# Kernel tuning notes

Measured on AMD Instinct MI355X. Metric: run time of the kernel, lower is better.

The kernel has to match this reference:

```python
import jax, jax.numpy as jnp
import numpy as np

NUM_USERS = 100000
NUM_ITEMS = 50000
N_NODES = NUM_USERS + NUM_ITEMS
LATENT_DIM = 64
XIJ_DIM = 16
N_LAYERS = 3
NNZ = 6400000
BATCH = 8192


def setup_inputs() -> dict:
    key = jax.random.key(0)
    ks = jax.random.split(key, 12)
    return {
        "emb_user": jax.random.normal(ks[0], (NUM_USERS, LATENT_DIM), jnp.float32),
        "emb_item": jax.random.normal(ks[1], (NUM_ITEMS, LATENT_DIM), jnp.float32),
        "emb_user_xij": jax.random.normal(ks[2], (NUM_USERS, XIJ_DIM), jnp.float32),
        "emb_item_xij1": jax.random.normal(ks[3], (NUM_ITEMS, XIJ_DIM), jnp.float32),
        "emb_item_xij0": jax.random.normal(ks[4], (NUM_ITEMS, XIJ_DIM), jnp.float32),
        "w_user": jax.random.normal(ks[5], (1,), jnp.float32),
        "w_item": jax.random.normal(ks[6], (1,), jnp.float32),
        "graph_vals": jax.random.uniform(ks[7], (NNZ,), jnp.float32),
        "graph_rows": jax.random.randint(ks[8], (NNZ,), 0, N_NODES, jnp.int64).astype(jnp.int32),
        "graph_cols": jax.random.randint(ks[9], (NNZ,), 0, N_NODES, jnp.int64).astype(jnp.int32),
        "users": jax.random.randint(ks[10], (BATCH,), 0, NUM_USERS, jnp.int64).astype(jnp.int32),
        "items": jax.random.randint(ks[11], (BATCH,), 0, NUM_ITEMS, jnp.int64).astype(jnp.int32),
        "xij": jax.random.randint(jax.random.fold_in(key, 99), (BATCH,), 0, 2, jnp.int32),
    }


def _spmm(rows, cols, vals, x):
    # y[r] = sum_{e: rows[e]==r} vals[e] * x[cols[e]]
    return jax.ops.segment_sum(vals[:, None] * x[cols], rows, num_segments=N_NODES)


def reference(emb_user, emb_item, emb_user_xij, emb_item_xij1, emb_item_xij0,
              w_user, w_item, graph_vals, graph_rows, graph_cols,
              users, items, xij):
    # LightGCN propagation with running-mean accumulator (fuses the stack+mean)
    all_emb = jnp.concatenate([emb_user, emb_item], axis=0)  # [N, D]
    acc = all_emb
    for _ in range(N_LAYERS):
        all_emb = _spmm(graph_rows, graph_cols, graph_vals, all_emb)
        acc = acc + all_emb
    light_out = acc / (N_LAYERS + 1)
    all_users = light_out[:NUM_USERS]
    all_items = light_out[NUM_USERS:]

    users_emb = w_user * all_users[users]          # [B, D]
    items_emb = w_item * all_items[items]          # [B, D]
    xij_user_emb = emb_user_xij[users]             # [B, Dx]
    xij_item_emb = jnp.where(xij[:, None].astype(bool),
                             emb_item_xij1[items], emb_item_xij0[items])

    users_mix = jax.nn.softmax(jnp.concatenate([users_emb, xij_user_emb], axis=1), axis=1)
    items_mix = jax.nn.sigmoid(jnp.concatenate([items_emb, xij_item_emb], axis=1))
    gamma = jnp.sum(users_mix * items_mix, axis=1)  # [B]
    return gamma
```

## Files before the change

kernel.cpp:

```cpp
#include <hip/hip_runtime.h>
#include <hip/hip_bf16.h>
#include <hip/hip_fp16.h>
#include <math.h>

#define NUM_USERS 100000
#define NUM_ITEMS 50000
#define N_NODES   150000
#define DIM       64
#define VAL_SCALE 16383.0f
#define VAL_INV   (1.0f / 16383.0f)

#define SSHIFT 9
#define SROWS  512
#define NBS    ((N_NODES + SROWS - 1) / SROWS)
#define CAP    17
#define FLUSH  8
#define SCAT_WGS 1280
#define GPAD   16
#define SLOTS  32768
#define PKSLOTS 22744
#define SENTINEL 0xFFFFFFFFu
#define BBT 512

__global__ void copy_init_kernel(const float4* __restrict__ eu, const float4* __restrict__ ei,
                                 ushort4* __restrict__ cur, int total4) {
    int i = blockIdx.x * blockDim.x + threadIdx.x;
    if (i >= total4) return;
    const int user_lim = NUM_USERS * (DIM / 4);
    float4 v = (i < user_lim) ? eu[i] : ei[i - user_lim];
    ushort4 h;
    h.x = __half_as_ushort(__float2half_rn(v.x));
    h.y = __half_as_ushort(__float2half_rn(v.y));
    h.z = __half_as_ushort(__float2half_rn(v.z));
    h.w = __half_as_ushort(__float2half_rn(v.w));
    cur[i] = h;
}

__global__ void gcur_init_kernel(int* __restrict__ gcur) {
    int b = blockIdx.x * blockDim.x + threadIdx.x;
    if (b < NBS) gcur[b * GPAD] = b * SLOTS;
}

__global__ __launch_bounds__(256) void binned_scatter_kernel(
        const int* __restrict__ rows, const int* __restrict__ cols,
        const float* __restrict__ vals, int* __restrict__ gcur,
        uint2* __restrict__ pk8, int nnz) {
    __shared__ unsigned       lbufA[NBS * CAP];
    __shared__ unsigned short lbufB[NBS * CAP];
    __shared__ int            lcur[NBS];
    int t = threadIdx.x;
    for (int i = t; i < NBS; i += 256) lcur[i] = 0;
    __syncthreads();

    int per_wg = (((nnz + (int)gridDim.x - 1) / (int)gridDim.x) + 1) & ~1;
    int e0 = blockIdx.x * per_wg;
    int e1 = min(e0 + per_wg, nnz);

    #define PROC(rr, cc, vv) { \
        int r = (rr); \
        unsigned q = __float2uint_rn((vv) * VAL_SCALE); \
        unsigned ax = (unsigned)(cc) | (q << 18); \
        int b = r >> SSHIFT; \
        int pos = atomicAdd(&lcur[b], 1); \
        if (pos < CAP) { \
            lbufA[b * CAP + pos] = ax; \
            lbufB[b * CAP + pos] = (unsigned short)(r - (b << SSHIFT)); \
        } else { \
            atomicSub(&lcur[b], 1); \
            int p = atomicAdd(&gcur[b * GPAD], 8); \
            *(uint4*)(&pk8[p])     = make_uint4(ax, (unsigned)r, 0u, SENTINEL); \
            *(uint4*)(&pk8[p + 2]) = make_uint4(0u, SENTINEL, 0u, SENTINEL); \
            *(uint4*)(&pk8[p + 4]) = make_uint4(0u, SENTINEL, 0u, SENTINEL); \
            *(uint4*)(&pk8[p + 6]) = make_uint4(0u, SENTINEL, 0u, SENTINEL); \
        } }

    for (int base = e0; base < e1; base += 512) {
        int e = base + t * 2;
        if (e + 1 < e1) {
            int2   r2 = *(const int2*)(rows + e);
            int2   c2 = *(const int2*)(cols + e);
            float2 v2 = *(const float2*)(vals + e);
            PROC(r2.x, c2.x, v2.x)
            PROC(r2.y, c2.y, v2.y)
        } else if (e < e1) {
            PROC(rows[e], cols[e], vals[e])
        }
        __syncthreads();
        for (int b2 = t; b2 < NBS; b2 += 256) {
            int c = lcur[b2];
            if (c >= FLUSH) {
                int ng = c >> 3;
                int p = atomicAdd(&gcur[b2 * GPAD], ng * 8);
                unsigned rbase = (unsigned)(b2 << SSHIFT);
                for (int j = 0; j < ng * 8; j += 2) {
                    uint4 q = make_uint4(lbufA[b2 * CAP + j],     rbase + lbufB[b2 * CAP + j],
                                         lbufA[b2 * CAP + j + 1], rbase + lbufB[b2 * CAP + j + 1]);
                    *(uint4*)(&pk8[p + j]) = q;
                }
                int rem = c - ng * 8;
                for (int j = 0; j < rem; ++j) {
                    lbufA[b2 * CAP + j] = lbufA[b2 * CAP + ng * 8 + j];
                    lbufB[b2 * CAP + j] = lbufB[b2 * CAP + ng * 8 + j];
                }
                lcur[b2] = rem;
            }
        }
        __syncthreads();
    }
    for (int b2 = t; b2 < NBS; b2 += 256) {
        int c = lcur[b2];
        if (c > 0) {
            int p = atomicAdd(&gcur[b2 * GPAD], 8);
            unsigned rbase = (unsigned)(b2 << SSHIFT);
            for (int j = 0; j < 8; j += 2) {
                unsigned a0 = (j     < c) ? lbufA[b2 * CAP + j]             : 0u;
                unsigned b0 = (j     < c) ? rbase + lbufB[b2 * CAP + j]     : SENTINEL;
                unsigned a1 = (j + 1 < c) ? lbufA[b2 * CAP + j + 1]         : 0u;
                unsigned b1 = (j + 1 < c) ? rbase + lbufB[b2 * CAP + j + 1] : SENTINEL;
                *(uint4*)(&pk8[p + j]) = make_uint4(a0, b0, a1, b1);
            }
        }
    }
}

__global__ __launch_bounds__(BBT) void bucket_build_kernel(const int* __restrict__ gcur,
                                                           const uint2* __restrict__ pk8,
                                                           unsigned* __restrict__ pk,
                                                           int* __restrict__ rowbeg,
                                                           int* __restrict__ rowend) {
    __shared__ int lc[SROWS];
    __shared__ int ps[SROWS];
    int b  = blockIdx.x;
    int r0 = b * SROWS;
    int nr = min(r0 + SROWS, N_NODES) - r0;
    int t  = threadIdx.x;
    lc[t] = 0;
    __syncthreads();

    const uint4* p4 = (const uint4*)pk8;
    int i0   = (b * SLOTS) >> 1;
    int iend = gcur[b * GPAD] >> 1;

    #define CNT(q) { \
        if ((q).y != SENTINEL) atomicAdd(&lc[(int)(q).y - r0], 1); \
        if ((q).w != SENTINEL) atomicAdd(&lc[(int)(q).w - r0], 1); }

    int i = i0 + t;
    for (; i + 3 * BBT < iend; i += 4 * BBT) {
        uint4 qa = p4[i], qb = p4[i + BBT], qc = p4[i + 2 * BBT], qd = p4[i + 3 * BBT];
        CNT(qa) CNT(qb) CNT(qc) CNT(qd)
    }
    for (; i < iend; i += BBT) { uint4 qa = p4[i]; CNT(qa) }
    __syncthreads();

    int c = lc[t];
    ps[t] = c;
    __syncthreads();
    #pragma unroll
    for (int off = 1; off < SROWS; off <<= 1) {
        int u = (t >= off) ? ps[t - off] : 0;
        __syncthreads();
        ps[t] += u;
        __syncthreads();
    }
    int base = b * PKSLOTS + ps[t] - c;
    if (t < nr) { rowbeg[r0 + t] = base; rowend[r0 + t] = base + c; }
    lc[t] = base;
    __syncthreads();

    #define PLC(q) { \
        if ((q).y != SENTINEL) { int p_ = atomicAdd(&lc[(int)(q).y - r0], 1); pk[p_] = (q).x; } \
        if ((q).w != SENTINEL) { int p_ = atomicAdd(&lc[(int)(q).w - r0], 1); pk[p_] = (q).z; } }

    i = i0 + t;
    for (; i + 3 * BBT < iend; i += 4 * BBT) {
        uint4 qa = p4[i], qb = p4[i + BBT], qc = p4[i + 2 * BBT], qd = p4[i + 3 * BBT];
        PLC(qa) PLC(qb) PLC(qc) PLC(qd)
    }
    for (; i < iend; i += BBT) { uint4 qa = p4[i]; PLC(qa) }
}

__device__ __forceinline__ float row_pull(const int* __restrict__ rowbeg,
                                          const int* __restrict__ rowend,
                                          const unsigned* __restrict__ pk,
                                          const __half* __restrict__ x,
                                          int row, int lane) {
    int s0 = rowbeg[row];
    int s1 = rowend[row];
    float acc = 0.f;
    int e = s0;
    for (; e + 16 <= s1; e += 16) {
        unsigned p0 = pk[e + 0],  p1 = pk[e + 1],  p2 = pk[e + 2],  p3 = pk[e + 3];
        unsigned p4 = pk[e + 4],  p5 = pk[e + 5],  p6 = pk[e + 6],  p7 = pk[e + 7];
        unsigned p8 = pk[e + 8],  p9 = pk[e + 9],  pA = pk[e + 10], pB = pk[e + 11];
        unsigned pC = pk[e + 12], pD = pk[e + 13], pE = pk[e + 14], pF = pk[e + 15];
        float x0 = __half2float(x[((p0 & 0x3FFFFu) << 6) + lane]);
        float x1 = __half2float(x[((p1 & 0x3FFFFu) << 6) + lane]);
        float x2 = __half2float(x[((p2 & 0x3FFFFu) << 6) + lane]);
        float x3 = __half2float(x[((p3 & 0x3FFFFu) << 6) + lane]);
        float x4 = __half2float(x[((p4 & 0x3FFFFu) << 6) + lane]);
        float x5 = __half2float(x[((p5 & 0x3FFFFu) << 6) + lane]);
        float x6 = __half2float(x[((p6 & 0x3FFFFu) << 6) + lane]);
        float x7 = __half2float(x[((p7 & 0x3FFFFu) << 6) + lane]);
        float x8 = __half2float(x[((p8 & 0x3FFFFu) << 6) + lane]);
        float x9 = __half2float(x[((p9 & 0x3FFFFu) << 6) + lane]);
        float xA = __half2float(x[((pA & 0x3FFFFu) << 6) + lane]);
        float xB = __half2float(x[((pB & 0x3FFFFu) << 6) + lane]);
        float xC = __half2float(x[((pC & 0x3FFFFu) << 6) + lane]);
        float xD = __half2float(x[((pD & 0x3FFFFu) << 6) + lane]);
        float xE = __half2float(x[((pE & 0x3FFFFu) << 6) + lane]);
        float xF = __half2float(x[((pF & 0x3FFFFu) << 6) + lane]);
        acc = fmaf((float)(p0 >> 18), x0, acc);
        acc = fmaf((float)(p1 >> 18), x1, acc);
        acc = fmaf((float)(p2 >> 18), x2, acc);
        acc = fmaf((float)(p3 >> 18), x3, acc);
        acc = fmaf((float)(p4 >> 18), x4, acc);
        acc = fmaf((float)(p5 >> 18), x5, acc);
        acc = fmaf((float)(p6 >> 18), x6, acc);
        acc = fmaf((float)(p7 >> 18), x7, acc);
        acc = fmaf((float)(p8 >> 18), x8, acc);
        acc = fmaf((float)(p9 >> 18), x9, acc);
        acc = fmaf((float)(pA >> 18), xA, acc);
        acc = fmaf((float)(pB >> 18), xB, acc);
        acc = fmaf((float)(pC >> 18), xC, acc);
        acc = fmaf((float)(pD >> 18), xD, acc);
        acc = fmaf((float)(pE >> 18), xE, acc);
        acc = fmaf((float)(pF >> 18), xF, acc);
    }
    for (; e + 8 <= s1; e += 8) {
        unsigned p0 = pk[e + 0], p1 = pk[e + 1], p2 = pk[e + 2], p3 = pk[e + 3];
        unsigned p4 = pk[e + 4], p5 = pk[e + 5], p6 = pk[e + 6], p7 = pk[e + 7];
        float x0 = __half2float(x[((p0 & 0x3FFFFu) << 6) + lane]);
        float x1 = __half2float(x[((p1 & 0x3FFFFu) << 6) + lane]);
        float x2 = __half2float(x[((p2 & 0x3FFFFu) << 6) + lane]);
        float x3 = __half2float(x[((p3 & 0x3FFFFu) << 6) + lane]);
        float x4 = __half2float(x[((p4 & 0x3FFFFu) << 6) + lane]);
        float x5 = __half2float(x[((p5 & 0x3FFFFu) << 6) + lane]);
        float x6 = __half2float(x[((p6 & 0x3FFFFu) << 6) + lane]);
        float x7 = __half2float(x[((p7 & 0x3FFFFu) << 6) + lane]);
        acc = fmaf((float)(p0 >> 18), x0, acc);
        acc = fmaf((float)(p1 >> 18), x1, acc);
        acc = fmaf((float)(p2 >> 18), x2, acc);
        acc = fmaf((float)(p3 >> 18), x3, acc);
        acc = fmaf((float)(p4 >> 18), x4, acc);
        acc = fmaf((float)(p5 >> 18), x5, acc);
        acc = fmaf((float)(p6 >> 18), x6, acc);
        acc = fmaf((float)(p7 >> 18), x7, acc);
    }
    for (; e < s1; ++e) {
        unsigned p = pk[e];
        acc = fmaf((float)(p >> 18), __half2float(x[((p & 0x3FFFFu) << 6) + lane]), acc);
    }
    return acc * VAL_INV;
}

__device__ __forceinline__ float pull_range(const unsigned* __restrict__ pk,
                                            const __half* __restrict__ x,
                                            int e, int s1, int lane, float acc) {
    for (; e + 8 <= s1; e += 8) {
        unsigned p0 = pk[e + 0], p1 = pk[e + 1], p2 = pk[e + 2], p3 = pk[e + 3];
        unsigned p4 = pk[e + 4], p5 = pk[e + 5], p6 = pk[e + 6], p7 = pk[e + 7];
        float x0 = __half2float(x[((p0 & 0x3FFFFu) << 6) + lane]);
        float x1 = __half2float(x[((p1 & 0x3FFFFu) << 6) + lane]);
        float x2 = __half2float(x[((p2 & 0x3FFFFu) << 6) + lane]);
        float x3 = __half2float(x[((p3 & 0x3FFFFu) << 6) + lane]);
        float x4 = __half2float(x[((p4 & 0x3FFFFu) << 6) + lane]);
        float x5 = __half2float(x[((p5 & 0x3FFFFu) << 6) + lane]);
        float x6 = __half2float(x[((p6 & 0x3FFFFu) << 6) + lane]);
        float x7 = __half2float(x[((p7 & 0x3FFFFu) << 6) + lane]);
        acc = fmaf((float)(p0 >> 18), x0, acc);
        acc = fmaf((float)(p1 >> 18), x1, acc);
        acc = fmaf((float)(p2 >> 18), x2, acc);
        acc = fmaf((float)(p3 >> 18), x3, acc);
        acc = fmaf((float)(p4 >> 18), x4, acc);
        acc = fmaf((float)(p5 >> 18), x5, acc);
        acc = fmaf((float)(p6 >> 18), x6, acc);
        acc = fmaf((float)(p7 >> 18), x7, acc);
    }
    for (; e < s1; ++e) {
        unsigned p = pk[e];
        acc = fmaf((float)(p >> 18), __half2float(x[((p & 0x3FFFFu) << 6) + lane]), acc);
    }
    return acc;
}

__global__ __launch_bounds__(256) void pull_kernel(const int* __restrict__ rowbeg,
                                                   const int* __restrict__ rowend,
                                                   const unsigned* __restrict__ pk,
                                                   const __half* __restrict__ x,
                                                   __half* __restrict__ y) {
    int lane = threadIdx.x & 63;
    int wv   = __builtin_amdgcn_readfirstlane(threadIdx.x >> 6);
    int row  = blockIdx.x * 4 + wv;
    if (row >= N_NODES) return;
    float acc = row_pull(rowbeg, rowend, pk, x, row, lane);
    y[((size_t)row << 6) + lane] = __float2half_rn(acc);
}

__global__ __launch_bounds__(256) void tail_kernel(const int* __restrict__ rowbeg,
                                                   const int* __restrict__ rowend,
                                                   const unsigned* __restrict__ pk,
                                                   const __half* __restrict__ cur,
                                                   const __half* __restrict__ nxt,
                                                   const float* __restrict__ eu,
                                                   const float* __restrict__ ei,
                                                   const float* __restrict__ exu,
                                                   const float* __restrict__ exi1,
                                                   const float* __restrict__ exi0,
                                                   const float* __restrict__ w_user,
                                                   const float* __restrict__ w_item,
                                                   const int* __restrict__ users,
                                                   const int* __restrict__ items,
                                                   const int* __restrict__ xijf,
                                                   float* __restrict__ out, int batch) {
    int lane = threadIdx.x & 63;
    int wv   = blockIdx.x * 4 + __builtin_amdgcn_readfirstlane(threadIdx.x >> 6);
    if (wv >= batch) return;
    int u    = users[wv];
    int it   = items[wv];
    int xf   = xijf[wv];
    int rowU = u;
    int rowI = NUM_USERS + it;

    int eA = rowbeg[rowU], sA = rowend[rowU];
    int eB = rowbeg[rowI], sB = rowend[rowI];
    float aU = 0.f, aI = 0.f;
    for (; eA + 8 <= sA && eB + 8 <= sB; eA += 8, eB += 8) {
        unsigned a0 = pk[eA + 0], a1 = pk[eA + 1], a2 = pk[eA + 2], a3 = pk[eA + 3];
        unsigned a4 = pk[eA + 4], a5 = pk[eA + 5], a6 = pk[eA + 6], a7 = pk[eA + 7];
        unsigned b0 = pk[eB + 0], b1 = pk[eB + 1], b2 = pk[eB + 2], b3 = pk[eB + 3];
        unsigned b4 = pk[eB + 4], b5 = pk[eB + 5], b6 = pk[eB + 6], b7 = pk[eB + 7];
        float xa0 = __half2float(cur[((a0 & 0x3FFFFu) << 6) + lane]);
        float xa1 = __half2float(cur[((a1 & 0x3FFFFu) << 6) + lane]);
        float xa2 = __half2float(cur[((a2 & 0x3FFFFu) << 6) + lane]);
        float xa3 = __half2float(cur[((a3 & 0x3FFFFu) << 6) + lane]);
        float xa4 = __half2float(cur[((a4 & 0x3FFFFu) << 6) + lane]);
        float xa5 = __half2float(cur[((a5 & 0x3FFFFu) << 6) + lane]);
        float xa6 = __half2float(cur[((a6 & 0x3FFFFu) << 6) + lane]);
        float xa7 = __half2float(cur[((a7 & 0x3FFFFu) << 6) + lane]);
        float xb0 = __half2float(cur[((b0 & 0x3FFFFu) << 6) + lane]);
        float xb1 = __half2float(cur[((b1 & 0x3FFFFu) << 6) + lane]);
        float xb2 = __half2float(cur[((b2 & 0x3FFFFu) << 6) + lane]);
        float xb3 = __half2float(cur[((b3 & 0x3FFFFu) << 6) + lane]);
        float xb4 = __half2float(cur[((b4 & 0x3FFFFu) << 6) + lane]);
        float xb5 = __half2float(cur[((b5 & 0x3FFFFu) << 6) + lane]);
        float xb6 = __half2float(cur[((b6 & 0x3FFFFu) << 6) + lane]);
        float xb7 = __half2float(cur[((b7 & 0x3FFFFu) << 6) + lane]);
        aU = fmaf((float)(a0 >> 18), xa0, aU);
        aU = fmaf((float)(a1 >> 18), xa1, aU);
        aU = fmaf((float)(a2 >> 18), xa2, aU);
        aU = fmaf((float)(a3 >> 18), xa3, aU);
        aU = fmaf((float)(a4 >> 18), xa4, aU);
        aU = fmaf((float)(a5 >> 18), xa5, aU);
        aU = fmaf((float)(a6 >> 18), xa6, aU);
        aU = fmaf((float)(a7 >> 18), xa7, aU);
        aI = fmaf((float)(b0 >> 18), xb0, aI);
        aI = fmaf((float)(b1 >> 18), xb1, aI);
        aI = fmaf((float)(b2 >> 18), xb2, aI);
        aI = fmaf((float)(b3 >> 18), xb3, aI);
        aI = fmaf((float)(b4 >> 18), xb4, aI);
        aI = fmaf((float)(b5 >> 18), xb5, aI);
        aI = fmaf((float)(b6 >> 18), xb6, aI);
        aI = fmaf((float)(b7 >> 18), xb7, aI);
    }
    aU = pull_range(pk, cur, eA, sA, lane, aU);
    aI = pull_range(pk, cur, eB, sB, lane, aI);
    float l3u = aU * VAL_INV;
    float l3i = aI * VAL_INV;

    float wu = w_user[0] * 0.25f;
    float wi = w_item[0] * 0.25f;

    float su = eu[((size_t)u  << 6) + lane]
             + __half2float(nxt[((size_t)rowU << 6) + lane])
             + __half2float(cur[((size_t)rowU << 6) + lane])
             + l3u;
    float si = ei[((size_t)it << 6) + lane]
             + __half2float(nxt[((size_t)rowI << 6) + lane])
             + __half2float(cur[((size_t)rowI << 6) + lane])
             + l3i;
    float ua = wu * su;
    float ia = wi * si;

    float ub = -INFINITY, ib = 0.f;
    if (lane < 16) {
        ub = exu[(size_t)u * 16 + lane];
        ib = xf ? exi1[(size_t)it * 16 + lane] : exi0[(size_t)it * 16 + lane];
    }

    float m = fmaxf(ua, ub);
    #pragma unroll
    for (int off = 32; off; off >>= 1) m = fmaxf(m, __shfl_xor(m, off));
    float ea = expf(ua - m);
    float eb = (lane < 16) ? expf(ub - m) : 0.f;
    float s = ea + eb;
    #pragma unroll
    for (int off = 32; off; off >>= 1) s += __shfl_xor(s, off);
    float inv = 1.f / s;

    float sa = 1.f / (1.f + expf(-ia));
    float sb = (lane < 16) ? 1.f / (1.f + expf(-ib)) : 0.f;

    float g = ea * inv * sa + eb * inv * sb;
    #pragma unroll
    for (int off = 32; off; off >>= 1) g += __shfl_xor(g, off);
    if (lane == 0) out[wv] = g;
}

extern "C" void kernel_launch(void* const* d_in, const int* in_sizes, int n_in,
                              void* d_out, int out_size, void* d_ws, size_t ws_size,
                              hipStream_t stream) {
    const float* emb_user = (const float*)d_in[0];
    const float* emb_item = (const float*)d_in[1];
    const float* exu      = (const float*)d_in[2];
    const float* exi1     = (const float*)d_in[3];
    const float* exi0     = (const float*)d_in[4];
    const float* w_user   = (const float*)d_in[5];
    const float* w_item   = (const float*)d_in[6];
    const float* gvals    = (const float*)d_in[7];
    const int*   grows    = (const int*)d_in[8];
    const int*   gcols    = (const int*)d_in[9];
    const int*   users    = (const int*)d_in[10];
    const int*   items    = (const int*)d_in[11];
    const int*   xijf     = (const int*)d_in[12];
    float*       out      = (float*)d_out;

    const int nnz   = in_sizes[7];
    const int batch = in_sizes[10];

    const size_t node_elems = (size_t)N_NODES * DIM;
    const size_t PK8_BYTES  = (size_t)NBS * SLOTS * 8;
    char* w = (char*)d_ws;
    uint2*    pk8   = (uint2*)w;
    __half*   cur   = (__half*)w;
    __half*   nxt   = cur + node_elems;
    w += PK8_BYTES;
    unsigned* pk     = (unsigned*)w;              w += (size_t)NBS * PKSLOTS * 4;
    int*      rowbeg = (int*)w;                   w += (size_t)N_NODES * 4;
    int*      rowend = (int*)w;                   w += (size_t)N_NODES * 4;
    int*      gcur   = (int*)w;                   w += (size_t)NBS * GPAD * 4;

    const int tb = 256;
    const int total4 = N_NODES * (DIM / 4);

    gcur_init_kernel<<<(NBS + tb - 1) / tb, tb, 0, stream>>>(gcur);
    binned_scatter_kernel<<<SCAT_WGS, 256, 0, stream>>>(grows, gcols, gvals, gcur, pk8, nnz);
    bucket_build_kernel<<<NBS, BBT, 0, stream>>>(gcur, pk8, pk, rowbeg, rowend);

    copy_init_kernel<<<(total4 + tb - 1) / tb, tb, 0, stream>>>(
        (const float4*)emb_user, (const float4*)emb_item, (ushort4*)cur, total4);

    const int pull_blocks = (N_NODES + 3) / 4;
    const int tail_blocks = (batch + 3) / 4;

    pull_kernel<<<pull_blocks, tb, 0, stream>>>(rowbeg, rowend, pk, cur, nxt);
    pull_kernel<<<pull_blocks, tb, 0, stream>>>(rowbeg, rowend, pk, nxt, cur);
    tail_kernel<<<tail_blocks, tb, 0, stream>>>(
        rowbeg, rowend, pk, cur, nxt, emb_user, emb_item,
        exu, exi1, exi0, w_user, w_item, users, items, xijf, out, batch);
}
```

Measured before the change: 515.8 us.

## Split staged edge buffer into separate col/val and 16-bit local-row arrays

Replaces the interleaved 8-byte (packed col/val, absolute row) staging records with two planar arrays: 32-bit packed col/val words and 16-bit bucket-local row offsets, using 0xFFFF as the padding sentinel. The count pass of bucket build now reads only the 2-byte row array, and the placement pass reads rows plus col/val, which cuts staging traffic from 8 to 6 bytes per edge. Scatter writes are regrouped into 16-byte stores per array. The placement loop loses its 4-way unroll, which may reduce memory-level parallelism.

```diff
diff --git a/kernel.cpp b/kernel.cpp
--- a/kernel.cpp
+++ b/kernel.cpp
@@ -19,7 +19,7 @@
 #define GPAD   16
 #define SLOTS  32768
 #define PKSLOTS 22744
-#define SENTINEL 0xFFFFFFFFu
+#define SENTR  0xFFFFu
 #define BBT 512
 
 __global__ void copy_init_kernel(const float4* __restrict__ eu, const float4* __restrict__ ei,
@@ -44,7 +44,8 @@
 __global__ __launch_bounds__(256) void binned_scatter_kernel(
         const int* __restrict__ rows, const int* __restrict__ cols,
         const float* __restrict__ vals, int* __restrict__ gcur,
-        uint2* __restrict__ pk8, int nnz) {
+        unsigned* __restrict__ axbuf, unsigned short* __restrict__ rowbuf,
+        int nnz) {
     __shared__ unsigned       lbufA[NBS * CAP];
     __shared__ unsigned short lbufB[NBS * CAP];
     __shared__ int            lcur[NBS];
@@ -68,10 +69,11 @@
         } else { \
             atomicSub(&lcur[b], 1); \
             int p = atomicAdd(&gcur[b * GPAD], 8); \
-            *(uint4*)(&pk8[p])     = make_uint4(ax, (unsigned)r, 0u, SENTINEL); \
-            *(uint4*)(&pk8[p + 2]) = make_uint4(0u, SENTINEL, 0u, SENTINEL); \
-            *(uint4*)(&pk8[p + 4]) = make_uint4(0u, SENTINEL, 0u, SENTINEL); \
-            *(uint4*)(&pk8[p + 6]) = make_uint4(0u, SENTINEL, 0u, SENTINEL); \
+            *(uint4*)(&axbuf[p])     = make_uint4(ax, 0u, 0u, 0u); \
+            *(uint4*)(&axbuf[p + 4]) = make_uint4(0u, 0u, 0u, 0u); \
+            *(uint4*)(&rowbuf[p])    = make_uint4( \
+                (unsigned)(r - (b << SSHIFT)) | 0xFFFF0000u, \
+                0xFFFFFFFFu, 0xFFFFFFFFu, 0xFFFFFFFFu); \
         } }
 
     for (int base = e0; base < e1; base += 512) {
@@ -91,11 +93,17 @@
             if (c >= FLUSH) {
                 int ng = c >> 3;
                 int p = atomicAdd(&gcur[b2 * GPAD], ng * 8);
-                unsigned rbase = (unsigned)(b2 << SSHIFT);
-                for (int j = 0; j < ng * 8; j += 2) {
-                    uint4 q = make_uint4(lbufA[b2 * CAP + j],     rbase + lbufB[b2 * CAP + j],
-                                         lbufA[b2 * CAP + j + 1], rbase + lbufB[b2 * CAP + j + 1]);
-                    *(uint4*)(&pk8[p + j]) = q;
+                for (int j = 0; j < ng * 8; j += 4) {
+                    *(uint4*)(&axbuf[p + j]) = make_uint4(
+                        lbufA[b2 * CAP + j],     lbufA[b2 * CAP + j + 1],
+                        lbufA[b2 * CAP + j + 2], lbufA[b2 * CAP + j + 3]);
+                }
+                for (int j = 0; j < ng * 8; j += 8) {
+                    unsigned w0 = (unsigned)lbufB[b2 * CAP + j]     | ((unsigned)lbufB[b2 * CAP + j + 1] << 16);
+                    unsigned w1 = (unsigned)lbufB[b2 * CAP + j + 2] | ((unsigned)lbufB[b2 * CAP + j + 3] << 16);
+                    unsigned w2 = (unsigned)lbufB[b2 * CAP + j + 4] | ((unsigned)lbufB[b2 * CAP + j + 5] << 16);
+                    unsigned w3 = (unsigned)lbufB[b2 * CAP + j + 6] | ((unsigned)lbufB[b2 * CAP + j + 7] << 16);
+                    *(uint4*)(&rowbuf[p + j]) = make_uint4(w0, w1, w2, w3);
                 }
                 int rem = c - ng * 8;
                 for (int j = 0; j < rem; ++j) {
@@ -111,20 +119,25 @@
         int c = lcur[b2];
         if (c > 0) {
             int p = atomicAdd(&gcur[b2 * GPAD], 8);
-            unsigned rbase = (unsigned)(b2 << SSHIFT);
-            for (int j = 0; j < 8; j += 2) {
-                unsigned a0 = (j     < c) ? lbufA[b2 * CAP + j]             : 0u;
-                unsigned b0 = (j     < c) ? rbase + lbufB[b2 * CAP + j]     : SENTINEL;
-                unsigned a1 = (j + 1 < c) ? lbufA[b2 * CAP + j + 1]         : 0u;
-                unsigned b1 = (j + 1 < c) ? rbase + lbufB[b2 * CAP + j + 1] : SENTINEL;
-                *(uint4*)(&pk8[p + j]) = make_uint4(a0, b0, a1, b1);
+            unsigned av[8]; unsigned rv[8];
+            #pragma unroll
+            for (int j = 0; j < 8; ++j) {
+                av[j] = (j < c) ? lbufA[b2 * CAP + j] : 0u;
+                rv[j] = (j < c) ? (unsigned)lbufB[b2 * CAP + j] : SENTR;
             }
+            *(uint4*)(&axbuf[p])     = make_uint4(av[0], av[1], av[2], av[3]);
+            *(uint4*)(&axbuf[p + 4]) = make_uint4(av[4], av[5], av[6], av[7]);
+            *(uint4*)(&rowbuf[p])    = make_uint4(rv[0] | (rv[1] << 16),
+                                                  rv[2] | (rv[3] << 16),
+                                                  rv[4] | (rv[5] << 16),
+                                                  rv[6] | (rv[7] << 16));
         }
     }
 }
 
 __global__ __launch_bounds__(BBT) void bucket_build_kernel(const int* __restrict__ gcur,
-                                                           const uint2* __restrict__ pk8,
+                                                           const unsigned* __restrict__ axbuf,
+                                                           const unsigned short* __restrict__ rowbuf,
                                                            unsigned* __restrict__ pk,
                                                            int* __restrict__ rowbeg,
                                                            int* __restrict__ rowend) {
@@ -137,20 +150,28 @@
     lc[t] = 0;
     __syncthreads();
 
-    const uint4* p4 = (const uint4*)pk8;
-    int i0   = (b * SLOTS) >> 1;
-    int iend = gcur[b * GPAD] >> 1;
-
-    #define CNT(q) { \
-        if ((q).y != SENTINEL) atomicAdd(&lc[(int)(q).y - r0], 1); \
-        if ((q).w != SENTINEL) atomicAdd(&lc[(int)(q).w - r0], 1); }
+    const uint4* r4 = (const uint4*)rowbuf;
+    const uint4* a4 = (const uint4*)axbuf;
+    int i0   = (b * SLOTS) >> 3;
+    int iend = gcur[b * GPAD] >> 3;
+
+    #define CNT8(q) { \
+        unsigned h; \
+        h = (q).x & 0xFFFFu; if (h != SENTR) atomicAdd(&lc[h], 1); \
+        h = (q).x >> 16;     if (h != SENTR) atomicAdd(&lc[h], 1); \
+        h = (q).y & 0xFFFFu; if (h != SENTR) atomicAdd(&lc[h], 1); \
+        h = (q).y >> 16;     if (h != SENTR) atomicAdd(&lc[h], 1); \
+        h = (q).z & 0xFFFFu; if (h != SENTR) atomicAdd(&lc[h], 1); \
+        h = (q).z >> 16;     if (h != SENTR) atomicAdd(&lc[h], 1); \
+        h = (q).w & 0xFFFFu; if (h != SENTR) atomicAdd(&lc[h], 1); \
+        h = (q).w >> 16;     if (h != SENTR) atomicAdd(&lc[h], 1); }
 
     int i = i0 + t;
-    for (; i + 3 * BBT < iend; i += 4 * BBT) {
-        uint4 qa = p4[i], qb = p4[i + BBT], qc = p4[i + 2 * BBT], qd = p4[i + 3 * BBT];
-        CNT(qa) CNT(qb) CNT(qc) CNT(qd)
-    }
-    for (; i < iend; i += BBT) { uint4 qa = p4[i]; CNT(qa) }
+    for (; i + BBT < iend; i += 2 * BBT) {
+        uint4 q1 = r4[i], q2 = r4[i + BBT];
+        CNT8(q1) CNT8(q2)
+    }
+    for (; i < iend; i += BBT) { uint4 q1 = r4[i]; CNT8(q1) }
     __syncthreads();
 
     int c = lc[t];
@@ -168,16 +189,22 @@
     lc[t] = base;
     __syncthreads();
 
-    #define PLC(q) { \
-        if ((q).y != SENTINEL) { int p_ = atomicAdd(&lc[(int)(q).y - r0], 1); pk[p_] = (q).x; } \
-        if ((q).w != SENTINEL) { int p_ = atomicAdd(&lc[(int)(q).w - r0], 1); pk[p_] = (q).z; } }
+    #define PLC2(h, v) { \
+        if ((h) != SENTR) { int p_ = atomicAdd(&lc[(h)], 1); pk[p_] = (v); } }
 
     i = i0 + t;
-    for (; i + 3 * BBT < iend; i += 4 * BBT) {
-        uint4 qa = p4[i], qb = p4[i + BBT], qc = p4[i + 2 * BBT], qd = p4[i + 3 * BBT];
-        PLC(qa) PLC(qb) PLC(qc) PLC(qd)
-    }
-    for (; i < iend; i += BBT) { uint4 qa = p4[i]; PLC(qa) }
+    for (; i < iend; i += BBT) {
+        uint4 rq = r4[i];
+        uint4 a0 = a4[2 * i], a1 = a4[2 * i + 1];
+        PLC2(rq.x & 0xFFFFu, a0.x)
+        PLC2(rq.x >> 16,     a0.y)
+        PLC2(rq.y & 0xFFFFu, a0.z)
+        PLC2(rq.y >> 16,     a0.w)
+        PLC2(rq.z & 0xFFFFu, a1.x)
+        PLC2(rq.z >> 16,     a1.y)
+        PLC2(rq.w & 0xFFFFu, a1.z)
+        PLC2(rq.w >> 16,     a1.w)
+    }
 }
 
 __device__ __forceinline__ float row_pull(const int* __restrict__ rowbeg,
@@ -428,24 +455,26 @@
     const int nnz   = in_sizes[7];
     const int batch = in_sizes[10];
 
-    const size_t node_elems = (size_t)N_NODES * DIM;
-    const size_t PK8_BYTES  = (size_t)NBS * SLOTS * 8;
+    const size_t node_elems  = (size_t)N_NODES * DIM;
+    const size_t STAGE_SLOTS = (size_t)NBS * SLOTS;
     char* w = (char*)d_ws;
-    uint2*    pk8   = (uint2*)w;
-    __half*   cur   = (__half*)w;
-    __half*   nxt   = cur + node_elems;
-    w += PK8_BYTES;
-    unsigned* pk     = (unsigned*)w;              w += (size_t)NBS * PKSLOTS * 4;
-    int*      rowbeg = (int*)w;                   w += (size_t)N_NODES * 4;
-    int*      rowend = (int*)w;                   w += (size_t)N_NODES * 4;
-    int*      gcur   = (int*)w;                   w += (size_t)NBS * GPAD * 4;
+    unsigned*       axbuf  = (unsigned*)w;
+    __half*         cur    = (__half*)w;
+    __half*         nxt    = cur + node_elems;
+    w += STAGE_SLOTS * 4;
+    unsigned short* rowbuf = (unsigned short*)w;  w += STAGE_SLOTS * 2;
+    unsigned*       pk     = (unsigned*)w;        w += (size_t)NBS * PKSLOTS * 4;
+    int*            rowbeg = (int*)w;             w += (size_t)N_NODES * 4;
+    int*            rowend = (int*)w;             w += (size_t)N_NODES * 4;
+    int*            gcur   = (int*)w;             w += (size_t)NBS * GPAD * 4;
 
     const int tb = 256;
     const int total4 = N_NODES * (DIM / 4);
 
     gcur_init_kernel<<<(NBS + tb - 1) / tb, tb, 0, stream>>>(gcur);
-    binned_scatter_kernel<<<SCAT_WGS, 256, 0, stream>>>(grows, gcols, gvals, gcur, pk8, nnz);
-    bucket_build_kernel<<<NBS, BBT, 0, stream>>>(gcur, pk8, pk, rowbeg, rowend);
+    binned_scatter_kernel<<<SCAT_WGS, 256, 0, stream>>>(grows, gcols, gvals, gcur,
+                                                        axbuf, rowbuf, nnz);
+    bucket_build_kernel<<<NBS, BBT, 0, stream>>>(gcur, axbuf, rowbuf, pk, rowbeg, rowend);
 
     copy_init_kernel<<<(total4 + tb - 1) / tb, tb, 0, stream>>>(
         (const float4*)emb_user, (const float4*)emb_item, (ushort4*)cur, total4);
```

Result: no change. 508.3 us (median of 3 runs) (-1.5%).
